# Performance work log

Hardware: AMD Instinct MI355X
Metric: run time of the kernel (lower is better)

## Reference

```python
import jax, jax.numpy as jnp
import numpy as np

B, CIN, H, W = 16, 3, 128, 128
C = 256          # out_channels
NH = 8           # num_heads
HD = C // NH     # head_dim = 32
SCALE = HD ** -0.5
EPS = 1e-5


def setup_inputs() -> dict:
    key = jax.random.key(0)
    ks = jax.random.split(key, 8)
    def xavier(k, fan_out, fan_in):
        lim = np.sqrt(6.0 / (fan_in + fan_out))
        return jax.random.uniform(k, (fan_out, fan_in), jnp.float32, -lim, lim)
    return {
        "x": jax.random.normal(ks[0], (B, CIN, H, W), jnp.float32),
        "Wi": xavier(ks[1], C, CIN),      # input_conv 1x1
        "bi": jnp.zeros((C,), jnp.float32),
        "Wqkv": xavier(ks[2], 3 * C, C),  # qkv_conv 1x1, no bias
        "Wo": xavier(ks[3], C, C),        # output_proj
        "bo": jnp.zeros((C,), jnp.float32),
        "Wf": xavier(ks[4], C, C),        # feature_update_conv
        "bf": jnp.zeros((C,), jnp.float32),
        "gamma": jnp.ones((C,), jnp.float32),
        "beta": jnp.zeros((C,), jnp.float32),
        "rmean": jnp.zeros((C,), jnp.float32),
        "rvar": jnp.ones((C,), jnp.float32),
    }


def reference(x, Wi, bi, Wqkv, Wo, bo, Wf, bf, gamma, beta, rmean, rvar):
    b, _, h, w = x.shape
    hw = h * w
    # input 1x1 conv
    x1 = jnp.einsum('oi,bihw->bohw', Wi, x) + bi[:, None, None]
    # qkv 1x1 conv, reshape (b, NH, 3, HD, h*w) matching torch channel layout
    qkv = jnp.einsum('oi,bihw->bohw', Wqkv, x1).reshape(b, NH, 3, HD, hw)
    q, k, v = qkv[:, :, 0], qkv[:, :, 1], qkv[:, :, 2]  # each (b, NH, HD, hw)
    # channel-channel attention: (b, NH, HD, HD), sigmoid gate (no softmax)
    attention = jax.nn.sigmoid(jnp.einsum('bndp,bnep->bnde', q, k) * SCALE)
    A = jnp.einsum('bnde,bnep->bndp', attention, v).reshape(b, C, h, w)
    A = jnp.einsum('oi,bihw->bohw', Wo, A) + bo[:, None, None]
    A = jnp.einsum('oi,bihw->bohw', Wf, A) + bf[:, None, None]
    # BatchNorm2d (eval mode: running stats)
    inv = gamma / jnp.sqrt(rvar + EPS)
    A = (A - rmean[:, None, None]) * inv[:, None, None] + beta[:, None, None]
    A = jax.nn.silu(A)  # dropout is identity in eval
    out = A + x1
    return (out, attention)
```

## Files before the change

### kernel.cpp

```cpp
#include <hip/hip_runtime.h>
#include <math.h>


#define HW 16384
#define NBATCH 16
static constexpr float SCALE_ = 0.17677669529663687f;
static constexpr float EPS_ = 1e-5f;

typedef float f32x4 __attribute__((ext_vector_type(4)));

#define WS_PART 0
#define WS_WFO  4096
#define WS_BFO  69632
#define WS_WB4  69888
#define WS_AQ   71168
#define WS_A4G  75776
#define WS_GG   92160

__device__ __forceinline__ float sigmoidf_(float z) {
  return 1.0f / (1.0f + __expf(-z));
}

__global__ __launch_bounds__(256) void k_prep(
    const float* __restrict__ x,
    const float* __restrict__ Wi, const float* __restrict__ bi,
    const float* __restrict__ Wqkv,
    const float* __restrict__ Wo, const float* __restrict__ bo,
    const float* __restrict__ Wf, const float* __restrict__ bf,
    float* __restrict__ part, float* __restrict__ Wfo,
    float* __restrict__ bfo, float* __restrict__ Wb4,
    float* __restrict__ aqg)
{
  const int bx = blockIdx.x;
  const int tid = threadIdx.x;
  if (bx < 256) {
    const int b = bx >> 4;
    const int pi = bx & 15;
    const int p0 = pi * 1024 + tid * 4;
    const float4 a0 = *reinterpret_cast<const float4*>(x + (size_t)(b * 3 + 0) * HW + p0);
    const float4 a1 = *reinterpret_cast<const float4*>(x + (size_t)(b * 3 + 1) * HW + p0);
    const float4 a2 = *reinterpret_cast<const float4*>(x + (size_t)(b * 3 + 2) * HW + p0);
    float v[9];
    v[0] = a0.x * a0.x + a0.y * a0.y + a0.z * a0.z + a0.w * a0.w;
    v[1] = a0.x * a1.x + a0.y * a1.y + a0.z * a1.z + a0.w * a1.w;
    v[2] = a0.x * a2.x + a0.y * a2.y + a0.z * a2.z + a0.w * a2.w;
    v[3] = a1.x * a1.x + a1.y * a1.y + a1.z * a1.z + a1.w * a1.w;
    v[4] = a1.x * a2.x + a1.y * a2.y + a1.z * a2.z + a1.w * a2.w;
    v[5] = a2.x * a2.x + a2.y * a2.y + a2.z * a2.z + a2.w * a2.w;
    v[6] = a0.x + a0.y + a0.z + a0.w;
    v[7] = a1.x + a1.y + a1.z + a1.w;
    v[8] = a2.x + a2.y + a2.z + a2.w;
    __shared__ float wred[4][9];
    const int lane = tid & 63, wid = tid >> 6;
#pragma unroll
    for (int k = 0; k < 9; ++k) {
      float s = v[k];
#pragma unroll
      for (int off = 32; off; off >>= 1) s += __shfl_down(s, off, 64);
      if (lane == 0) wred[wid][k] = s;
    }
    __syncthreads();
    if (tid < 9) {
      part[bx * 9 + tid] = wred[0][tid] + wred[1][tid] + wred[2][tid] + wred[3][tid];
    }
  } else if (bx < 512) {
    const int o = bx - 256;
    const float* wfr = Wf + (size_t)o * 256;
    const int i = tid;
    float acc = 0.f;
#pragma unroll 32
    for (int k = 0; k < 256; ++k) acc = fmaf(wfr[k], Wo[(size_t)k * 256 + i], acc);
    Wfo[(size_t)o * 256 + i] = acc;
  } else if (bx == 512) {
    Wb4[tid * 4 + 0] = Wi[tid * 3 + 0];
    Wb4[tid * 4 + 1] = Wi[tid * 3 + 1];
    Wb4[tid * 4 + 2] = Wi[tid * 3 + 2];
    Wb4[tid * 4 + 3] = bi[tid];
    float acc = bf[tid];
    const float* wfr = Wf + (size_t)tid * 256;
#pragma unroll 16
    for (int k = 0; k < 256; ++k) acc = fmaf(wfr[k], bo[k], acc);
    bfo[tid] = acc;
  } else {
    const int blk = bx - 513;
    const int rl = tid >> 2;
    const int ch = tid & 3;
    const int row = blk * 64 + rl;
    const float* wr = Wqkv + (size_t)row * 256 + ch * 64;
    float c0 = 0, c1 = 0, c2 = 0, c3 = 0;
#pragma unroll 8
    for (int c = 0; c < 64; ++c) {
      const float w = wr[c];
      const int cc = ch * 64 + c;
      c0 = fmaf(w, Wi[cc * 3 + 0], c0);
      c1 = fmaf(w, Wi[cc * 3 + 1], c1);
      c2 = fmaf(w, Wi[cc * 3 + 2], c2);
      c3 = fmaf(w, bi[cc], c3);
    }
    __shared__ float red[64][4][4];
    red[rl][ch][0] = c0; red[rl][ch][1] = c1;
    red[rl][ch][2] = c2; red[rl][ch][3] = c3;
    __syncthreads();
    const int j = tid & 3;
    aqg[(size_t)(blk * 64 + rl) * 4 + j] =
        red[rl][0][j] + red[rl][1][j] + red[rl][2][j] + red[rl][3][j];
  }
}

__global__ __launch_bounds__(256) void k_solveA(
    const float* __restrict__ part, const float* __restrict__ aqg,
    float* __restrict__ att_out,
    float* __restrict__ A4g)
{
  const int n = blockIdx.x;
  const int b = blockIdx.y;
  const int tid = threadIdx.x;
  __shared__ float Ms[9];
  __shared__ float aqh[96][5];
  __shared__ float att_s[32][33];
  if (tid < 9) {
    float s = 0.f;
    for (int j = 0; j < 16; ++j) s += part[(b * 16 + j) * 9 + tid];
    Ms[tid] = s;
  }
  if (tid < 96) {
    const float4 v = *reinterpret_cast<const float4*>(aqg + (size_t)(n * 96 + tid) * 4);
    aqh[tid][0] = v.x; aqh[tid][1] = v.y; aqh[tid][2] = v.z; aqh[tid][3] = v.w;
  }
  __syncthreads();
  const float M00 = Ms[0], M01 = Ms[1], M02 = Ms[2], M11 = Ms[3], M12 = Ms[4], M22 = Ms[5];
  const float s0 = Ms[6], s1 = Ms[7], s2 = Ms[8];
#pragma unroll
  for (int r = 0; r < 4; ++r) {
    const int idx = tid + r * 256;
    const int d = idx >> 5, e = idx & 31;
    const float* q = aqh[d];
    const float* k = aqh[32 + e];
    const float q0 = q[0], q1 = q[1], q2 = q[2], q3 = q[3];
    const float k0 = k[0], k1 = k[1], k2 = k[2], k3 = k[3];
    const float t = q0 * (M00 * k0 + M01 * k1 + M02 * k2)
                  + q1 * (M01 * k0 + M11 * k1 + M12 * k2)
                  + q2 * (M02 * k0 + M12 * k1 + M22 * k2)
                  + q3 * (s0 * k0 + s1 * k1 + s2 * k2)
                  + k3 * (s0 * q0 + s1 * q1 + s2 * q2)
                  + 16384.0f * q3 * k3;
    const float a = sigmoidf_(SCALE_ * t);
    att_s[d][e] = a;
    att_out[(size_t)(b * 8 + n) * 1024 + idx] = a;
  }
  __syncthreads();
  if (tid < 128) {
    const int d = tid >> 2, j = tid & 3;
    float acc = 0.f;
#pragma unroll 8
    for (int e = 0; e < 32; ++e) acc = fmaf(att_s[d][e], aqh[64 + e][j], acc);
    A4g[(size_t)(b * 256 + n * 32 + d) * 4 + j] = acc;
  }
}

__global__ __launch_bounds__(256) void k_fold(
    const float* __restrict__ Wfo, const float* __restrict__ bfo,
    const float* __restrict__ A4g,
    const float* __restrict__ gamma, const float* __restrict__ beta,
    const float* __restrict__ rmean, const float* __restrict__ rvar,
    float* __restrict__ Gg)
{
  const int c0 = blockIdx.x * 32;
  const int b = blockIdx.y;
  const int tid = threadIdx.x;
  __shared__ float4 A4v[256];
  __shared__ float Wfo_s[32][257];
  __shared__ float4 partial[32][9];

  A4v[tid] = *reinterpret_cast<const float4*>(A4g + ((size_t)b * 256 + tid) * 4);
#pragma unroll
  for (int it = 0; it < 8; ++it) {
    const int idx = tid + it * 256;
    const int r = idx >> 6, kq = idx & 63;
    const float4 v = *reinterpret_cast<const float4*>(
        Wfo + ((size_t)(c0 + r) * 256 + kq * 4));
    Wfo_s[r][kq * 4 + 0] = v.x; Wfo_s[r][kq * 4 + 1] = v.y;
    Wfo_s[r][kq * 4 + 2] = v.z; Wfo_s[r][kq * 4 + 3] = v.w;
  }
  __syncthreads();
  {
    const int ks = tid >> 5, o = tid & 31;
    float4 acc = make_float4(0.f, 0.f, 0.f, 0.f);
#pragma unroll 8
    for (int i = 0; i < 32; ++i) {
      const float w = Wfo_s[o][ks * 32 + i];
      const float4 a = A4v[ks * 32 + i];
      acc.x = fmaf(w, a.x, acc.x); acc.y = fmaf(w, a.y, acc.y);
      acc.z = fmaf(w, a.z, acc.z); acc.w = fmaf(w, a.w, acc.w);
    }
    partial[o][ks] = acc;
  }
  __syncthreads();
  if (tid < 32) {
    const int o = tid;
    float4 s = partial[o][0];
#pragma unroll
    for (int k2 = 1; k2 < 8; ++k2) {
      const float4 p = partial[o][k2];
      s.x += p.x; s.y += p.y; s.z += p.z; s.w += p.w;
    }
    const int c = c0 + o;
    const float inv = gamma[c] / sqrtf(rvar[c] + EPS_);
    const float g3 = (s.w + bfo[c] - rmean[c]) * inv + beta[c];
    *reinterpret_cast<float4*>(Gg + (size_t)(b * 256 + c) * 4) =
        make_float4(s.x * inv, s.y * inv, s.z * inv, g3);
  }
}

__global__ __launch_bounds__(256) void k_final(
    const float* __restrict__ x,
    const float4* __restrict__ Gg4,
    const float4* __restrict__ Wb4,
    float* __restrict__ out)
{
  const int c = blockIdx.x;
  const int b = blockIdx.y;
  const float4 g = Gg4[b * 256 + c];
  const float4 w = Wb4[c];
  const float* xb = x + (size_t)b * 3 * HW;
  float* ob = out + ((size_t)b * 256 + c) * HW;
  const int t4 = threadIdx.x * 4;
#pragma unroll 4
  for (int it = 0; it < 16; ++it) {
    const int p = it * 1024 + t4;
    const float4 X0 = *reinterpret_cast<const float4*>(xb + p);
    const float4 X1 = *reinterpret_cast<const float4*>(xb + HW + p);
    const float4 X2 = *reinterpret_cast<const float4*>(xb + 2 * HW + p);
    f32x4 r;
    {
      const float y = fmaf(g.x, X0.x, fmaf(g.y, X1.x, fmaf(g.z, X2.x, g.w)));
      r.x = y * sigmoidf_(y) + fmaf(w.x, X0.x, fmaf(w.y, X1.x, fmaf(w.z, X2.x, w.w)));
    }
    {
      const float y = fmaf(g.x, X0.y, fmaf(g.y, X1.y, fmaf(g.z, X2.y, g.w)));
      r.y = y * sigmoidf_(y) + fmaf(w.x, X0.y, fmaf(w.y, X1.y, fmaf(w.z, X2.y, w.w)));
    }
    {
      const float y = fmaf(g.x, X0.z, fmaf(g.y, X1.z, fmaf(g.z, X2.z, g.w)));
      r.z = y * sigmoidf_(y) + fmaf(w.x, X0.z, fmaf(w.y, X1.z, fmaf(w.z, X2.z, w.w)));
    }
    {
      const float y = fmaf(g.x, X0.w, fmaf(g.y, X1.w, fmaf(g.z, X2.w, g.w)));
      r.w = y * sigmoidf_(y) + fmaf(w.x, X0.w, fmaf(w.y, X1.w, fmaf(w.z, X2.w, w.w)));
    }
    __builtin_nontemporal_store(r, reinterpret_cast<f32x4*>(ob + p));
  }
}

extern "C" void kernel_launch(void* const* d_in, const int* in_sizes, int n_in,
                              void* d_out, int out_size, void* d_ws, size_t ws_size,
                              hipStream_t stream) {
  const float* x     = (const float*)d_in[0];
  const float* Wi    = (const float*)d_in[1];
  const float* bi    = (const float*)d_in[2];
  const float* Wqkv  = (const float*)d_in[3];
  const float* Wo    = (const float*)d_in[4];
  const float* bo    = (const float*)d_in[5];
  const float* Wf    = (const float*)d_in[6];
  const float* bf    = (const float*)d_in[7];
  const float* gamma = (const float*)d_in[8];
  const float* beta  = (const float*)d_in[9];
  const float* rmean = (const float*)d_in[10];
  const float* rvar  = (const float*)d_in[11];

  float* out = (float*)d_out;
  float* att = out + (size_t)NBATCH * 256 * HW;
  float* wsf = (float*)d_ws;

  k_prep<<<dim3(525), dim3(256), 0, stream>>>(x, Wi, bi, Wqkv, Wo, bo, Wf, bf,
                                              wsf + WS_PART, wsf + WS_WFO,
                                              wsf + WS_BFO, wsf + WS_WB4,
                                              wsf + WS_AQ);
  k_solveA<<<dim3(8, NBATCH), dim3(256), 0, stream>>>(wsf + WS_PART, wsf + WS_AQ,
                                                      att, wsf + WS_A4G);
  k_fold<<<dim3(8, NBATCH), dim3(256), 0, stream>>>(wsf + WS_WFO, wsf + WS_BFO,
                                                    wsf + WS_A4G, gamma, beta,
                                                    rmean, rvar, wsf + WS_GG);
  k_final<<<dim3(256, NBATCH), dim3(256), 0, stream>>>(
      x, (const float4*)(wsf + WS_GG), (const float4*)(wsf + WS_WB4), out);
}
```

Before: 76.56 us.

## Reuse input pixels across 32 channels per block in final kernel

k_final now loads each thread's three input-channel float4 values once and loops over 32 output channels. The per-channel g/w coefficients are staged in shared memory, so the x rereads that previously happened for every output channel are avoided. The grid becomes 16x8x16 blocks, and each thread writes 32 strided rows. The sigmoid also switches to the hardware reciprocal instruction, which is slightly less precise.

```diff
diff --git a/kernel.cpp b/kernel.cpp
--- a/kernel.cpp
+++ b/kernel.cpp
@@ -18,7 +18,7 @@
 #define WS_GG   92160
 
 __device__ __forceinline__ float sigmoidf_(float z) {
-  return 1.0f / (1.0f + __expf(-z));
+  return __builtin_amdgcn_rcpf(1.0f + __expf(-z));
 }
 
 __global__ __launch_bounds__(256) void k_prep(
@@ -218,19 +218,22 @@
     const float4* __restrict__ Wb4,
     float* __restrict__ out)
 {
-  const int c = blockIdx.x;
-  const int b = blockIdx.y;
-  const float4 g = Gg4[b * 256 + c];
-  const float4 w = Wb4[c];
-  const float* xb = x + (size_t)b * 3 * HW;
-  float* ob = out + ((size_t)b * 256 + c) * HW;
-  const int t4 = threadIdx.x * 4;
-#pragma unroll 4
-  for (int it = 0; it < 16; ++it) {
-    const int p = it * 1024 + t4;
-    const float4 X0 = *reinterpret_cast<const float4*>(xb + p);
-    const float4 X1 = *reinterpret_cast<const float4*>(xb + HW + p);
-    const float4 X2 = *reinterpret_cast<const float4*>(xb + 2 * HW + p);
+  const int b = blockIdx.z;
+  const int c0 = blockIdx.y * 32;
+  const int tid = threadIdx.x;
+  __shared__ float4 sg[32], sw[32];
+  if (tid < 32) sg[tid] = Gg4[b * 256 + c0 + tid];
+  else if (tid < 64) sw[tid - 32] = Wb4[c0 + tid - 32];
+  __syncthreads();
+  const int p4 = (blockIdx.x * 256 + tid) * 4;
+  const float4 X0 = *reinterpret_cast<const float4*>(x + (size_t)(b * 3 + 0) * HW + p4);
+  const float4 X1 = *reinterpret_cast<const float4*>(x + (size_t)(b * 3 + 1) * HW + p4);
+  const float4 X2 = *reinterpret_cast<const float4*>(x + (size_t)(b * 3 + 2) * HW + p4);
+  float* ob = out + (size_t)(b * 256 + c0) * HW + p4;
+#pragma unroll 2
+  for (int ci = 0; ci < 32; ++ci) {
+    const float4 g = sg[ci];
+    const float4 w = sw[ci];
     f32x4 r;
     {
       const float y = fmaf(g.x, X0.x, fmaf(g.y, X1.x, fmaf(g.z, X2.x, g.w)));
@@ -248,7 +251,8 @@
       const float y = fmaf(g.x, X0.w, fmaf(g.y, X1.w, fmaf(g.z, X2.w, g.w)));
       r.w = y * sigmoidf_(y) + fmaf(w.x, X0.w, fmaf(w.y, X1.w, fmaf(w.z, X2.w, w.w)));
     }
-    __builtin_nontemporal_store(r, reinterpret_cast<f32x4*>(ob + p));
+    __builtin_nontemporal_store(r, reinterpret_cast<f32x4*>(ob));
+    ob += HW;
   }
 }
 
@@ -281,6 +285,6 @@
   k_fold<<<dim3(8, NBATCH), dim3(256), 0, stream>>>(wsf + WS_WFO, wsf + WS_BFO,
                                                     wsf + WS_A4G, gamma, beta,
                                                     rmean, rvar, wsf + WS_GG);
-  k_final<<<dim3(256, NBATCH), dim3(256), 0, stream>>>(
+  k_final<<<dim3(16, 8, NBATCH), dim3(256), 0, stream>>>(
       x, (const float4*)(wsf + WS_GG), (const float4*)(wsf + WS_WB4), out);
 }
```

Result: no change. 75.82 us (-1.0%).
